# Kernel optimization log

Hardware: AMD Instinct MI355X
Metric: run time of the kernel (lower is better)

The kernel has to match this reference:

```python
import jax, jax.numpy as jnp
import numpy as np

P = 5          # config.num_pillars
H = 64         # config.hidden_dim // 4
B = 262144     # batch of pillar vectors
LN_EPS = 1e-5  # torch LayerNorm default eps
NORM_EPS = 1e-12  # F.normalize default eps


def _potential(x, W1, b1, W2, b2):
    # potential_net: Linear(P,H) -> GELU(exact) -> Linear(H,1)
    h = jax.nn.gelu(x @ W1 + b1, approximate=False)
    return h @ W2 + b2  # [..., 1]


def _layernorm(x, g, b):
    mu = x.mean(-1, keepdims=True)
    var = x.var(-1, keepdims=True)  # biased, matches torch LayerNorm
    return (x - mu) / jnp.sqrt(var + LN_EPS) * g + b


def setup_inputs() -> dict:
    key = jax.random.key(0)
    ks = jax.random.split(key, 8)
    s = lambda k, shape, scale: (jax.random.normal(k, shape, jnp.float32) * scale)
    return {
        "pillars": jax.random.uniform(ks[0], (B, P), jnp.float32),
        "W1": s(ks[1], (P, H), 1.0 / np.sqrt(P)),
        "b1": s(ks[2], (H,), 0.01),
        "W2": s(ks[3], (H, 1), 1.0 / np.sqrt(H)),
        "b2": s(ks[4], (1,), 0.01),
        "ln_gamma": jnp.ones((P,), jnp.float32),
        "ln_beta": jnp.zeros((P,), jnp.float32),
        "Wc": s(ks[5], (2 * P + 2, 1), 1.0 / np.sqrt(2 * P + 2)),
        "bc": s(ks[6], (1,), 0.01),
    }


def reference(pillars, W1, b1, W2, b2, ln_gamma, ln_beta, Wc, bc):
    # detect_catastrophe_batch path (includes compute_hessian_eigenvalues)
    p = jnp.clip(jnp.nan_to_num(pillars, nan=0.5), 0.0, 1.0)

    # V(p) and dV/dp  (batched; replaces per-call autograd.grad)
    V = _potential(p, W1, b1, W2, b2)  # [B,1]
    grad = jax.grad(lambda q: _potential(q, W1, b1, W2, b2).sum())(p)  # [B,P]

    # compute_hessian_eigenvalues: stabilize, per-sample 5x5 Hessian, eigvalsh
    x = _layernorm(p, ln_gamma, ln_beta)  # [B,P]
    pot_scalar = lambda xi: _potential(xi, W1, b1, W2, b2)[0]
    Hm = jax.vmap(jax.hessian(pot_scalar))(x)  # [B,P,P]
    Hm = 0.5 * (Hm + jnp.swapaxes(Hm, -1, -2))  # symmetrize (as in source)
    ev = jnp.linalg.eigvalsh(Hm)  # [B,P] ascending, matches torch.linalg.eigvalsh
    e_mean = ev.mean(-1, keepdims=True)  # [B,1]

    # features -> L2 normalize -> classifier -> clamp
    feats = jnp.concatenate([pillars, grad, V, e_mean], axis=-1)  # [B,2P+2]
    feats = feats / jnp.maximum(
        jnp.linalg.norm(feats, axis=-1, keepdims=True), NORM_EPS
    )
    probs = jnp.clip(jax.nn.sigmoid(feats @ Wc + bc), 0.0, 1.0)  # [B,1]
    return probs
```

## Files before the change

kernel.cpp:

```cpp
#include <hip/hip_runtime.h>
#include <math.h>

#define NP 5
#define NH 64
#define NPAIR 32
#define BLK 256

typedef float f32x2 __attribute__((ext_vector_type(2)));
typedef float f32x4 __attribute__((ext_vector_type(4)));

#define LOG2E 1.44269504088896340736f
#define C_CDF0 2.30220840f
#define C_CDF1 0.10294324f
#define C_G2A 1.59576912f
#define C_G2B 0.21406460f
#define C_PDF_A (-0.72134752f)
#define C_PDF_B (-1.32574806f)

__global__ __launch_bounds__(BLK) void topo_kernel(
    const float* __restrict__ pillars,
    const float* __restrict__ gW1,
    const float* __restrict__ gb1,
    const float* __restrict__ gW2,
    const float* __restrict__ gb2,
    const float* __restrict__ gLng,
    const float* __restrict__ gLnb,
    const float* __restrict__ gWc,
    const float* __restrict__ gbc,
    float* __restrict__ out,
    int n)
{
    __shared__ float sPack[NPAIR * 16];
    __shared__ float sGam[NP], sBet[NP], sWc[12], sScal[2];
    __shared__ float sPil[BLK * NP];

    const int t = threadIdx.x;
    if (t < NH) {
        float w0 = gW1[t],        w1 = gW1[NH + t], w2 = gW1[2*NH + t];
        float w3 = gW1[3*NH + t], w4 = gW1[4*NH + t];
        float bb = gb1[t], wo = gW2[t];
        float s  = w0*w0 + w1*w1 + w2*w2 + w3*w3 + w4*w4;
        float sw = 0.2f * s * wo;
        const int base = (t >> 1) * 16 + (t & 1);
        sPack[base + 0]  = w0;  sPack[base + 2]  = w1;
        sPack[base + 4]  = w2;  sPack[base + 6]  = w3;
        sPack[base + 8]  = w4;  sPack[base + 10] = bb;
        sPack[base + 12] = wo;  sPack[base + 14] = sw;
    } else if (t >= 64 && t < 64 + NP) {
        int j = t - 64; sGam[j] = gLng[j]; sBet[j] = gLnb[j];
    } else if (t >= 96 && t < 108) {
        int j = t - 96; sWc[j] = gWc[j];
    } else if (t == 128) { sScal[0] = gb2[0]; }
    else if (t == 129)   { sScal[1] = gbc[0]; }

    const long base = (long)blockIdx.x * BLK;
    const long gbp = base * NP;
    const long total = (long)n * NP;
    for (int i = t; i < BLK * NP; i += BLK) {
        long gi = gbp + i;
        sPil[i] = (gi < total) ? pillars[gi] : 0.f;
    }
    __syncthreads();

    const long sidx = base + t;
    if (sidx >= n) return;

    float raw[NP], p[NP], x[NP];
    #pragma unroll
    for (int j = 0; j < NP; ++j) raw[j] = sPil[t * NP + j];

    float mu = 0.f;
    #pragma unroll
    for (int j = 0; j < NP; ++j) {
        float v = raw[j];
        if (!(v == v)) v = 0.5f;
        v = fminf(fmaxf(v, 0.f), 1.f);
        p[j] = v; mu += v;
    }
    mu *= 0.2f;
    float var = 0.f;
    #pragma unroll
    for (int j = 0; j < NP; ++j) { float d = p[j] - mu; var += d * d; }
    var *= 0.2f;
    float inv = rsqrtf(var + 1e-5f);
    #pragma unroll
    for (int j = 0; j < NP; ++j) x[j] = (p[j] - mu) * inv * sGam[j] + sBet[j];

    f32x2 P[NP], X[NP];
    #pragma unroll
    for (int j = 0; j < NP; ++j) { P[j] = (f32x2){p[j], p[j]}; X[j] = (f32x2){x[j], x[j]}; }

    const f32x2 one = {1.f, 1.f}, two = {2.f, 2.f};
    const f32x2 cC0 = {-C_CDF0, -C_CDF0}, cC1 = {-C_CDF1, -C_CDF1};
    const f32x2 cGA = {C_G2A, C_G2A},     cGB = {C_G2B, C_G2B};
    const f32x2 cPA = {C_PDF_A, C_PDF_A}, cPB = {C_PDF_B, C_PDF_B};

    f32x2 V2 = {0.f,0.f}, TR = {0.f,0.f};
    f32x2 G0 = {0.f,0.f}, G1 = {0.f,0.f}, G2 = {0.f,0.f}, G3 = {0.f,0.f}, G4 = {0.f,0.f};

    const f32x4* pk4 = reinterpret_cast<const f32x4*>(sPack);
    #pragma unroll 4
    for (int pp = 0; pp < NPAIR; ++pp) {
        f32x4 q0 = pk4[pp * 4 + 0];
        f32x4 q1 = pk4[pp * 4 + 1];
        f32x4 q2 = pk4[pp * 4 + 2];
        f32x4 q3 = pk4[pp * 4 + 3];
        f32x2 w0 = q0.xy, w1 = q0.zw;
        f32x2 w2 = q1.xy, w3 = q1.zw;
        f32x2 w4 = q2.xy, bb = q2.zw;
        f32x2 wo = q3.xy, sw = q3.zw;

        f32x2 z  = P[0]*w0 + (P[1]*w1 + (P[2]*w2 + (P[3]*w3 + (P[4]*w4 + bb))));
        f32x2 zx = X[0]*w0 + (X[1]*w1 + (X[2]*w2 + (X[3]*w3 + (X[4]*w4 + bb))));

        f32x2 tz = z * z;
        f32x2 tx = zx * zx;

        f32x2 ya = z * (tz * cC1 + cC0);
        f32x2 e;
        e.x = __builtin_amdgcn_exp2f(ya.x);
        e.y = __builtin_amdgcn_exp2f(ya.y);
        f32x2 ope = e + one;
        f32x2 s;
        s.x = __builtin_amdgcn_rcpf(ope.x);
        s.y = __builtin_amdgcn_rcpf(ope.y);

        V2 = (z * s) * wo + V2;
        f32x2 u   = s - s * s;
        f32x2 g2p = tz * cGB + cGA;
        f32x2 d1  = ((z * u) * g2p + s) * wo;
        G0 = w0 * d1 + G0; G1 = w1 * d1 + G1; G2 = w2 * d1 + G2;
        G3 = w3 * d1 + G3; G4 = w4 * d1 + G4;

        f32x2 pa = tx * cPA + cPB;
        f32x2 ph;
        ph.x = __builtin_amdgcn_exp2f(pa.x);
        ph.y = __builtin_amdgcn_exp2f(pa.y);
        TR = (sw * (two - tx)) * ph + TR;
    }

    float V = V2.x + V2.y + sScal[0];
    float emean = TR.x + TR.y;

    float f[12];
    f[0] = raw[0]; f[1] = raw[1]; f[2] = raw[2]; f[3] = raw[3]; f[4] = raw[4];
    f[5] = G0.x + G0.y; f[6] = G1.x + G1.y; f[7] = G2.x + G2.y;
    f[8] = G3.x + G3.y; f[9] = G4.x + G4.y;
    f[10] = V; f[11] = emean;

    float nrm = 0.f;
    #pragma unroll
    for (int i = 0; i < 12; ++i) nrm = fmaf(f[i], f[i], nrm);
    float denom = fmaxf(sqrtf(nrm), 1e-12f);
    float dot = 0.f;
    #pragma unroll
    for (int i = 0; i < 12; ++i) dot = fmaf(f[i], sWc[i], dot);
    float sarg = dot * __builtin_amdgcn_rcpf(denom) + sScal[1];
    float es = __builtin_amdgcn_exp2f(-sarg * LOG2E);
    float prob = __builtin_amdgcn_rcpf(1.0f + es);
    prob = fminf(fmaxf(prob, 0.f), 1.f);
    out[sidx] = prob;
}

extern "C" void kernel_launch(void* const* d_in, const int* in_sizes, int n_in,
                              void* d_out, int out_size, void* d_ws, size_t ws_size,
                              hipStream_t stream) {
    const float* pillars = (const float*)d_in[0];
    const float* W1  = (const float*)d_in[1];
    const float* b1  = (const float*)d_in[2];
    const float* W2  = (const float*)d_in[3];
    const float* b2  = (const float*)d_in[4];
    const float* lng = (const float*)d_in[5];
    const float* lnb = (const float*)d_in[6];
    const float* Wc  = (const float*)d_in[7];
    const float* bc  = (const float*)d_in[8];
    float* out = (float*)d_out;

    const int n = in_sizes[0] / NP;
    const int blocks = (n + BLK - 1) / BLK;
    topo_kernel<<<blocks, BLK, 0, stream>>>(
        pillars, W1, b1, W2, b2, lng, lnb, Wc, bc, out, n);
}
```

Baseline: 19.76 us.

## Precompute packed weights in a prep kernel and stream them via scalar loads

A tiny prep kernel packs the weights into the workspace. The main kernel then reads them with double-buffered s_load_dwordx16 scalar loads instead of per-block LDS staging. The LDS pillar staging and the __syncthreads are removed, and each thread reads its pillars directly from global memory. This cuts LDS traffic and the per-block barrier and prologue, but adds a second kernel launch, uncoalesced strided pillar loads, and hand-written asm waits that limit how the compiler can schedule.

```diff
diff --git a/kernel.cpp b/kernel.cpp
--- a/kernel.cpp
+++ b/kernel.cpp
@@ -3,11 +3,10 @@
 
 #define NP 5
 #define NH 64
-#define NPAIR 32
 #define BLK 256
 
-typedef float f32x2 __attribute__((ext_vector_type(2)));
-typedef float f32x4 __attribute__((ext_vector_type(4)));
+typedef float f32x2  __attribute__((ext_vector_type(2)));
+typedef float f32x16 __attribute__((ext_vector_type(16)));
 
 #define LOG2E 1.44269504088896340736f
 #define C_CDF0 2.30220840f
@@ -17,57 +16,55 @@
 #define C_PDF_A (-0.72134752f)
 #define C_PDF_B (-1.32574806f)
 
+__global__ __launch_bounds__(64) void prep_kernel(
+    const float* __restrict__ gW1, const float* __restrict__ gb1,
+    const float* __restrict__ gW2, const float* __restrict__ gb2,
+    const float* __restrict__ gLng, const float* __restrict__ gLnb,
+    const float* __restrict__ gWc, const float* __restrict__ gbc,
+    float* __restrict__ ws)
+{
+    const int k = threadIdx.x;
+    float w0 = gW1[k],        w1 = gW1[NH + k], w2 = gW1[2*NH + k];
+    float w3 = gW1[3*NH + k], w4 = gW1[4*NH + k];
+    float bb = gb1[k], wo = gW2[k];
+    float s  = w0*w0 + w1*w1 + w2*w2 + w3*w3 + w4*w4;
+    float sw = 0.2f * s * wo;
+    const int base = (k >> 1) * 16 + (k & 1);
+    ws[base + 0]  = w0;  ws[base + 2]  = w1;
+    ws[base + 4]  = w2;  ws[base + 6]  = w3;
+    ws[base + 8]  = w4;  ws[base + 10] = bb;
+    ws[base + 12] = wo;  ws[base + 14] = sw;
+    if (k < NP)  { ws[512 + k] = gLng[k]; ws[517 + k] = gLnb[k]; }
+    if (k < 12)  ws[522 + k] = gWc[k];
+    if (k == 0)  { ws[534] = gb2[0]; ws[535] = gbc[0]; }
+}
+
+#define SLOAD(Q, OFF) \
+    asm volatile("s_load_dwordx16 %0, %1, %2" : "=&s"(Q) : "s"(wsp), "n"(OFF))
+#define SWAIT() do { asm volatile("s_waitcnt lgkmcnt(0)" ::: "memory"); \
+    __builtin_amdgcn_sched_barrier(0); } while (0)
+
 __global__ __launch_bounds__(BLK) void topo_kernel(
     const float* __restrict__ pillars,
-    const float* __restrict__ gW1,
-    const float* __restrict__ gb1,
-    const float* __restrict__ gW2,
-    const float* __restrict__ gb2,
-    const float* __restrict__ gLng,
-    const float* __restrict__ gLnb,
-    const float* __restrict__ gWc,
-    const float* __restrict__ gbc,
+    const float* __restrict__ ws,
     float* __restrict__ out,
     int n)
 {
-    __shared__ float sPack[NPAIR * 16];
-    __shared__ float sGam[NP], sBet[NP], sWc[12], sScal[2];
-    __shared__ float sPil[BLK * NP];
-
     const int t = threadIdx.x;
-    if (t < NH) {
-        float w0 = gW1[t],        w1 = gW1[NH + t], w2 = gW1[2*NH + t];
-        float w3 = gW1[3*NH + t], w4 = gW1[4*NH + t];
-        float bb = gb1[t], wo = gW2[t];
-        float s  = w0*w0 + w1*w1 + w2*w2 + w3*w3 + w4*w4;
-        float sw = 0.2f * s * wo;
-        const int base = (t >> 1) * 16 + (t & 1);
-        sPack[base + 0]  = w0;  sPack[base + 2]  = w1;
-        sPack[base + 4]  = w2;  sPack[base + 6]  = w3;
-        sPack[base + 8]  = w4;  sPack[base + 10] = bb;
-        sPack[base + 12] = wo;  sPack[base + 14] = sw;
-    } else if (t >= 64 && t < 64 + NP) {
-        int j = t - 64; sGam[j] = gLng[j]; sBet[j] = gLnb[j];
-    } else if (t >= 96 && t < 108) {
-        int j = t - 96; sWc[j] = gWc[j];
-    } else if (t == 128) { sScal[0] = gb2[0]; }
-    else if (t == 129)   { sScal[1] = gbc[0]; }
-
-    const long base = (long)blockIdx.x * BLK;
-    const long gbp = base * NP;
-    const long total = (long)n * NP;
-    for (int i = t; i < BLK * NP; i += BLK) {
-        long gi = gbp + i;
-        sPil[i] = (gi < total) ? pillars[gi] : 0.f;
-    }
-    __syncthreads();
-
-    const long sidx = base + t;
+    const long sidx = (long)blockIdx.x * BLK + t;
     if (sidx >= n) return;
 
+    float gam[NP], bet[NP], wcf[12];
+    #pragma unroll
+    for (int j = 0; j < NP; ++j) { gam[j] = ws[512 + j]; bet[j] = ws[517 + j]; }
+    #pragma unroll
+    for (int i = 0; i < 12; ++i) wcf[i] = ws[522 + i];
+    const float b2v = ws[534], bcv = ws[535];
+
+    const float* prow = pillars + sidx * NP;
     float raw[NP], p[NP], x[NP];
     #pragma unroll
-    for (int j = 0; j < NP; ++j) raw[j] = sPil[t * NP + j];
+    for (int j = 0; j < NP; ++j) raw[j] = prow[j];
 
     float mu = 0.f;
     #pragma unroll
@@ -84,7 +81,7 @@
     var *= 0.2f;
     float inv = rsqrtf(var + 1e-5f);
     #pragma unroll
-    for (int j = 0; j < NP; ++j) x[j] = (p[j] - mu) * inv * sGam[j] + sBet[j];
+    for (int j = 0; j < NP; ++j) x[j] = (p[j] - mu) * inv * gam[j] + bet[j];
 
     f32x2 P[NP], X[NP];
     #pragma unroll
@@ -98,48 +95,54 @@
     f32x2 V2 = {0.f,0.f}, TR = {0.f,0.f};
     f32x2 G0 = {0.f,0.f}, G1 = {0.f,0.f}, G2 = {0.f,0.f}, G3 = {0.f,0.f}, G4 = {0.f,0.f};
 
-    const f32x4* pk4 = reinterpret_cast<const f32x4*>(sPack);
-    #pragma unroll 4
-    for (int pp = 0; pp < NPAIR; ++pp) {
-        f32x4 q0 = pk4[pp * 4 + 0];
-        f32x4 q1 = pk4[pp * 4 + 1];
-        f32x4 q2 = pk4[pp * 4 + 2];
-        f32x4 q3 = pk4[pp * 4 + 3];
-        f32x2 w0 = q0.xy, w1 = q0.zw;
-        f32x2 w2 = q1.xy, w3 = q1.zw;
-        f32x2 w4 = q2.xy, bb = q2.zw;
-        f32x2 wo = q3.xy, sw = q3.zw;
+    const float* wsp = ws;
+    f32x16 qA, qB;
+    SLOAD(qA, 0);
 
-        f32x2 z  = P[0]*w0 + (P[1]*w1 + (P[2]*w2 + (P[3]*w3 + (P[4]*w4 + bb))));
-        f32x2 zx = X[0]*w0 + (X[1]*w1 + (X[2]*w2 + (X[3]*w3 + (X[4]*w4 + bb))));
+#define BODY(Q)                                                              \
+    do {                                                                     \
+        f32x2 w0 = {Q[0],Q[1]},  w1 = {Q[2],Q[3]},  w2 = {Q[4],Q[5]};        \
+        f32x2 w3 = {Q[6],Q[7]},  w4 = {Q[8],Q[9]},  bb = {Q[10],Q[11]};      \
+        f32x2 wo = {Q[12],Q[13]}, sw = {Q[14],Q[15]};                        \
+        f32x2 z  = P[0]*w0 + (P[1]*w1 + (P[2]*w2 + (P[3]*w3 + (P[4]*w4 + bb)))); \
+        f32x2 zx = X[0]*w0 + (X[1]*w1 + (X[2]*w2 + (X[3]*w3 + (X[4]*w4 + bb)))); \
+        f32x2 tz = z * z;                                                    \
+        f32x2 tx = zx * zx;                                                  \
+        f32x2 ya = z * (tz * cC1 + cC0);                                     \
+        f32x2 e;                                                             \
+        e.x = __builtin_amdgcn_exp2f(ya.x);                                  \
+        e.y = __builtin_amdgcn_exp2f(ya.y);                                  \
+        f32x2 ope = e + one;                                                 \
+        f32x2 s;                                                             \
+        s.x = __builtin_amdgcn_rcpf(ope.x);                                  \
+        s.y = __builtin_amdgcn_rcpf(ope.y);                                  \
+        V2 = (z * s) * wo + V2;                                              \
+        f32x2 u   = s - s * s;                                               \
+        f32x2 g2p = tz * cGB + cGA;                                          \
+        f32x2 d1  = ((z * u) * g2p + s) * wo;                                \
+        G0 = w0 * d1 + G0; G1 = w1 * d1 + G1; G2 = w2 * d1 + G2;             \
+        G3 = w3 * d1 + G3; G4 = w4 * d1 + G4;                                \
+        f32x2 pa = tx * cPA + cPB;                                           \
+        f32x2 ph;                                                            \
+        ph.x = __builtin_amdgcn_exp2f(pa.x);                                 \
+        ph.y = __builtin_amdgcn_exp2f(pa.y);                                 \
+        TR = (sw * (two - tx)) * ph + TR;                                    \
+    } while (0)
 
-        f32x2 tz = z * z;
-        f32x2 tx = zx * zx;
+    #pragma unroll
+    for (int pp = 0; pp < 32; ++pp) {
+        SWAIT();
+        if (pp & 1) {
+            if (pp < 31) SLOAD(qA, ((pp + 1) * 64));
+            BODY(qB);
+        } else {
+            if (pp < 31) SLOAD(qB, ((pp + 1) * 64));
+            BODY(qA);
+        }
+    }
+#undef BODY
 
-        f32x2 ya = z * (tz * cC1 + cC0);
-        f32x2 e;
-        e.x = __builtin_amdgcn_exp2f(ya.x);
-        e.y = __builtin_amdgcn_exp2f(ya.y);
-        f32x2 ope = e + one;
-        f32x2 s;
-        s.x = __builtin_amdgcn_rcpf(ope.x);
-        s.y = __builtin_amdgcn_rcpf(ope.y);
-
-        V2 = (z * s) * wo + V2;
-        f32x2 u   = s - s * s;
-        f32x2 g2p = tz * cGB + cGA;
-        f32x2 d1  = ((z * u) * g2p + s) * wo;
-        G0 = w0 * d1 + G0; G1 = w1 * d1 + G1; G2 = w2 * d1 + G2;
-        G3 = w3 * d1 + G3; G4 = w4 * d1 + G4;
-
-        f32x2 pa = tx * cPA + cPB;
-        f32x2 ph;
-        ph.x = __builtin_amdgcn_exp2f(pa.x);
-        ph.y = __builtin_amdgcn_exp2f(pa.y);
-        TR = (sw * (two - tx)) * ph + TR;
-    }
-
-    float V = V2.x + V2.y + sScal[0];
+    float V = V2.x + V2.y + b2v;
     float emean = TR.x + TR.y;
 
     float f[12];
@@ -154,8 +157,8 @@
     float denom = fmaxf(sqrtf(nrm), 1e-12f);
     float dot = 0.f;
     #pragma unroll
-    for (int i = 0; i < 12; ++i) dot = fmaf(f[i], sWc[i], dot);
-    float sarg = dot * __builtin_amdgcn_rcpf(denom) + sScal[1];
+    for (int i = 0; i < 12; ++i) dot = fmaf(f[i], wcf[i], dot);
+    float sarg = dot * __builtin_amdgcn_rcpf(denom) + bcv;
     float es = __builtin_amdgcn_exp2f(-sarg * LOG2E);
     float prob = __builtin_amdgcn_rcpf(1.0f + es);
     prob = fminf(fmaxf(prob, 0.f), 1.f);
@@ -175,9 +178,11 @@
     const float* Wc  = (const float*)d_in[7];
     const float* bc  = (const float*)d_in[8];
     float* out = (float*)d_out;
+    float* ws  = (float*)d_ws;
+
+    prep_kernel<<<1, 64, 0, stream>>>(W1, b1, W2, b2, lng, lnb, Wc, bc, ws);
 
     const int n = in_sizes[0] / NP;
     const int blocks = (n + BLK - 1) / BLK;
-    topo_kernel<<<blocks, BLK, 0, stream>>>(
-        pillars, W1, b1, W2, b2, lng, lnb, Wc, bc, out, n);
+    topo_kernel<<<blocks, BLK, 0, stream>>>(pillars, ws, out, n);
 }
```

Measured after the change: 22.79 us. 15.3% more time.

## Drop shared-memory staging; read weights and pillars directly from global memory

Applied to the files above, without the earlier changes.

Removes the LDS staging of packed weights, LayerNorm/classifier params and the block's pillar rows, along with the __syncthreads barrier. Each thread now loads its pillar row directly and reads W1/b1/W2 through uniform global (scalar) loads, recomputing the per-unit squared-norm term inside the loop. This aims to cut LDS traffic and barrier latency, and lets the weight loads become scalar-cache reads. In exchange it adds strided per-thread global loads for the pillars, which coalesce less well, plus a few extra VALU ops per hidden pair.

```diff
diff --git a/kernel.cpp b/kernel.cpp
--- a/kernel.cpp
+++ b/kernel.cpp
@@ -3,11 +3,9 @@
 
 #define NP 5
 #define NH 64
-#define NPAIR 32
 #define BLK 256
 
 typedef float f32x2 __attribute__((ext_vector_type(2)));
-typedef float f32x4 __attribute__((ext_vector_type(4)));
 
 #define LOG2E 1.44269504088896340736f
 #define C_CDF0 2.30220840f
@@ -30,44 +28,21 @@
     float* __restrict__ out,
     int n)
 {
-    __shared__ float sPack[NPAIR * 16];
-    __shared__ float sGam[NP], sBet[NP], sWc[12], sScal[2];
-    __shared__ float sPil[BLK * NP];
-
     const int t = threadIdx.x;
-    if (t < NH) {
-        float w0 = gW1[t],        w1 = gW1[NH + t], w2 = gW1[2*NH + t];
-        float w3 = gW1[3*NH + t], w4 = gW1[4*NH + t];
-        float bb = gb1[t], wo = gW2[t];
-        float s  = w0*w0 + w1*w1 + w2*w2 + w3*w3 + w4*w4;
-        float sw = 0.2f * s * wo;
-        const int base = (t >> 1) * 16 + (t & 1);
-        sPack[base + 0]  = w0;  sPack[base + 2]  = w1;
-        sPack[base + 4]  = w2;  sPack[base + 6]  = w3;
-        sPack[base + 8]  = w4;  sPack[base + 10] = bb;
-        sPack[base + 12] = wo;  sPack[base + 14] = sw;
-    } else if (t >= 64 && t < 64 + NP) {
-        int j = t - 64; sGam[j] = gLng[j]; sBet[j] = gLnb[j];
-    } else if (t >= 96 && t < 108) {
-        int j = t - 96; sWc[j] = gWc[j];
-    } else if (t == 128) { sScal[0] = gb2[0]; }
-    else if (t == 129)   { sScal[1] = gbc[0]; }
-
-    const long base = (long)blockIdx.x * BLK;
-    const long gbp = base * NP;
-    const long total = (long)n * NP;
-    for (int i = t; i < BLK * NP; i += BLK) {
-        long gi = gbp + i;
-        sPil[i] = (gi < total) ? pillars[gi] : 0.f;
-    }
-    __syncthreads();
-
-    const long sidx = base + t;
+    const long sidx = (long)blockIdx.x * BLK + t;
     if (sidx >= n) return;
 
+    float gam[NP], bet[NP], wcf[12];
+    #pragma unroll
+    for (int j = 0; j < NP; ++j) { gam[j] = gLng[j]; bet[j] = gLnb[j]; }
+    #pragma unroll
+    for (int i = 0; i < 12; ++i) wcf[i] = gWc[i];
+    const float b2v = gb2[0], bcv = gbc[0];
+
+    const float* prow = pillars + sidx * NP;
     float raw[NP], p[NP], x[NP];
     #pragma unroll
-    for (int j = 0; j < NP; ++j) raw[j] = sPil[t * NP + j];
+    for (int j = 0; j < NP; ++j) raw[j] = prow[j];
 
     float mu = 0.f;
     #pragma unroll
@@ -84,7 +59,7 @@
     var *= 0.2f;
     float inv = rsqrtf(var + 1e-5f);
     #pragma unroll
-    for (int j = 0; j < NP; ++j) x[j] = (p[j] - mu) * inv * sGam[j] + sBet[j];
+    for (int j = 0; j < NP; ++j) x[j] = (p[j] - mu) * inv * gam[j] + bet[j];
 
     f32x2 P[NP], X[NP];
     #pragma unroll
@@ -98,17 +73,19 @@
     f32x2 V2 = {0.f,0.f}, TR = {0.f,0.f};
     f32x2 G0 = {0.f,0.f}, G1 = {0.f,0.f}, G2 = {0.f,0.f}, G3 = {0.f,0.f}, G4 = {0.f,0.f};
 
-    const f32x4* pk4 = reinterpret_cast<const f32x4*>(sPack);
     #pragma unroll 4
-    for (int pp = 0; pp < NPAIR; ++pp) {
-        f32x4 q0 = pk4[pp * 4 + 0];
-        f32x4 q1 = pk4[pp * 4 + 1];
-        f32x4 q2 = pk4[pp * 4 + 2];
-        f32x4 q3 = pk4[pp * 4 + 3];
-        f32x2 w0 = q0.xy, w1 = q0.zw;
-        f32x2 w2 = q1.xy, w3 = q1.zw;
-        f32x2 w4 = q2.xy, bb = q2.zw;
-        f32x2 wo = q3.xy, sw = q3.zw;
+    for (int pp = 0; pp < 32; ++pp) {
+        const int k0 = 2 * pp;
+        f32x2 w0 = {gW1[0*NH + k0], gW1[0*NH + k0 + 1]};
+        f32x2 w1 = {gW1[1*NH + k0], gW1[1*NH + k0 + 1]};
+        f32x2 w2 = {gW1[2*NH + k0], gW1[2*NH + k0 + 1]};
+        f32x2 w3 = {gW1[3*NH + k0], gW1[3*NH + k0 + 1]};
+        f32x2 w4 = {gW1[4*NH + k0], gW1[4*NH + k0 + 1]};
+        f32x2 bb = {gb1[k0], gb1[k0 + 1]};
+        f32x2 wo = {gW2[k0], gW2[k0 + 1]};
+
+        f32x2 ssum = w0*w0 + (w1*w1 + (w2*w2 + (w3*w3 + w4*w4)));
+        f32x2 sw = ssum * wo;
 
         f32x2 z  = P[0]*w0 + (P[1]*w1 + (P[2]*w2 + (P[3]*w3 + (P[4]*w4 + bb))));
         f32x2 zx = X[0]*w0 + (X[1]*w1 + (X[2]*w2 + (X[3]*w3 + (X[4]*w4 + bb))));
@@ -139,8 +116,8 @@
         TR = (sw * (two - tx)) * ph + TR;
     }
 
-    float V = V2.x + V2.y + sScal[0];
-    float emean = TR.x + TR.y;
+    float V = V2.x + V2.y + b2v;
+    float emean = 0.2f * (TR.x + TR.y);
 
     float f[12];
     f[0] = raw[0]; f[1] = raw[1]; f[2] = raw[2]; f[3] = raw[3]; f[4] = raw[4];
@@ -154,8 +131,8 @@
     float denom = fmaxf(sqrtf(nrm), 1e-12f);
     float dot = 0.f;
     #pragma unroll
-    for (int i = 0; i < 12; ++i) dot = fmaf(f[i], sWc[i], dot);
-    float sarg = dot * __builtin_amdgcn_rcpf(denom) + sScal[1];
+    for (int i = 0; i < 12; ++i) dot = fmaf(f[i], wcf[i], dot);
+    float sarg = dot * __builtin_amdgcn_rcpf(denom) + bcv;
     float es = __builtin_amdgcn_exp2f(-sarg * LOG2E);
     float prob = __builtin_amdgcn_rcpf(1.0f + es);
     prob = fminf(fmaxf(prob, 0.f), 1.f);
```

Result: faster. 19.10 us (median of 2 runs) (-3.3%).
